# Kernel tuning notes

Measured on AMD Instinct MI355X. Metric: run time of the kernel, lower is better.

Reference implementation:

```python
import jax, jax.numpy as jnp
import numpy as np

CHEB_K = 2  # hops per support; stacked terms = 1 + 2*CHEB_K = 5


def setup_inputs() -> dict:
    key = jax.random.key(0)
    k1, k2, k3, k4, k5 = jax.random.split(key, 5)
    B, N, C, O, D = 16, 1024, 64, 64, 10
    return {
        "x": jax.random.normal(k1, (B, N, C), dtype=jnp.float32),
        "adj": jax.random.uniform(k2, (2, B, N, N), dtype=jnp.float32),
        "node_embedding": jax.random.normal(k3, (N, D), dtype=jnp.float32),
        "weights_pool": jax.random.normal(k4, (D, 2 * CHEB_K + 1, C, O), dtype=jnp.float32) * 0.1,
        "bias_pool": jax.random.normal(k5, (D, O), dtype=jnp.float32) * 0.1,
    }


def reference(x, adj, node_embedding, weights_pool, bias_pool):
    # k-hop graph aggregation over each of the 2 supports
    out = [x]
    for s in range(adj.shape[0]):
        a = adj[s]  # [B, N, N]
        x1 = x
        for _ in range(CHEB_K):
            x1 = jnp.einsum('bnm,bmc->bnc', a, x1)
            out.append(x1)
    x_g = jnp.stack(out, axis=2)  # [B, N, K, C] with K = 2*cheb_k+1 (already node-major)
    # per-node hypernetwork weights and bias from node embeddings
    weights = jnp.einsum('nd,dkio->nkio', node_embedding, weights_pool)  # [N, K, C, O]
    bias = node_embedding @ bias_pool  # [N, O]
    # per-node contraction over (K, C)
    return jnp.einsum('bnki,nkio->bno', x_g, weights) + bias
```

## Files before the change

### kernel.cpp

```cpp
#include <hip/hip_runtime.h>
#include <stdint.h>


typedef __attribute__((ext_vector_type(4))) float f32x4;
typedef __attribute__((ext_vector_type(2))) float f32x2;
typedef __attribute__((ext_vector_type(8))) short s16x8;
typedef __attribute__((ext_vector_type(8))) __bf16 bf16x8;

__device__ __forceinline__ unsigned short f2bf(float f) {
  union { float f; uint32_t u; } v; v.f = f;
  uint32_t r = v.u + 0x7FFFu + ((v.u >> 16) & 1u);
  return (unsigned short)(r >> 16);
}
__device__ __forceinline__ uint32_t pack2(float a, float b) {
  return (uint32_t)f2bf(a) | ((uint32_t)f2bf(b) << 16);
}

union FragU { s16x8 s; bf16x8 b; };

__global__ void transpose_x(const float* __restrict__ x,
                            unsigned short* __restrict__ XT0) {
  __shared__ unsigned short tl[64][72];
  const int b = blockIdx.y, n0 = blockIdx.x * 64;
  const int tid = threadIdx.x;
  {
    const int c4 = (tid & 15) * 4;
#pragma unroll
    for (int i = 0; i < 4; ++i) {
      const int row = (tid >> 4) + i * 16;
      f32x4 v = *(const f32x4*)(x + ((size_t)(b * 1024 + n0 + row)) * 64 + c4);
      *(uint32_t*)&tl[row][c4]     = pack2(v[0], v[1]);
      *(uint32_t*)&tl[row][c4 + 2] = pack2(v[2], v[3]);
    }
  }
  __syncthreads();
  {
    const int c = tid >> 2;
    const int nch = (tid & 3) * 16;
    s16x8 s0, s1;
#pragma unroll
    for (int j = 0; j < 8; ++j) {
      s0[j] = (short)tl[nch + j][c];
      s1[j] = (short)tl[nch + 8 + j][c];
    }
    unsigned short* p = XT0 + (size_t)(b * 64 + c) * 1024 + n0 + nch;
    *(s16x8*)p = s0;
    *(s16x8*)(p + 8) = s1;
  }
}

__global__ void transpose_wp(const float* __restrict__ wp,
                             float* __restrict__ wpT) {
  __shared__ float tl[64][65];
  const int d = blockIdx.y;
  const int ki0 = blockIdx.x * 64;
  const int tid = threadIdx.x;
  const float* src = wp + (size_t)d * 20480;
  {
    const int o4 = (tid & 15) * 4;
#pragma unroll
    for (int i = 0; i < 4; ++i) {
      const int row = (tid >> 4) + i * 16;
      f32x4 v = *(const f32x4*)(src + (size_t)(ki0 + row) * 64 + o4);
      tl[row][o4] = v[0]; tl[row][o4 + 1] = v[1];
      tl[row][o4 + 2] = v[2]; tl[row][o4 + 3] = v[3];
    }
  }
  __syncthreads();
  {
    const int o = tid >> 2;
    const int kch = (tid & 3) * 16;
    float* dst = wpT + (size_t)d * 20480 + (size_t)o * 320 + ki0 + kch;
#pragma unroll
    for (int u = 0; u < 4; ++u) {
      f32x4 v = { tl[kch + 4 * u][o], tl[kch + 4 * u + 1][o],
                  tl[kch + 4 * u + 2][o], tl[kch + 4 * u + 3][o] };
      *(f32x4*)(dst + 4 * u) = v;
    }
  }
}

__global__ __launch_bounds__(256) void wgen(const float* __restrict__ wpT,
                                            const float* __restrict__ emb,
                                            unsigned short* __restrict__ WT) {
  const int idx = blockIdx.x * 256 + threadIdx.x;
  const int n0 = blockIdx.y * 16;
  float wv[10];
#pragma unroll
  for (int d = 0; d < 10; ++d) wv[d] = wpT[(size_t)d * 20480 + idx];
#pragma unroll
  for (int g = 0; g < 16; ++g) {
    float a = 0.f;
#pragma unroll
    for (int d = 0; d < 10; ++d) a += emb[(n0 + g) * 10 + d] * wv[d];
    WT[(size_t)(n0 + g) * 20480 + idx] = f2bf(a);
  }
}

#define PF 4
__global__ __launch_bounds__(256, 2) void hop_kernel(
    const float* __restrict__ adj, const unsigned short* __restrict__ XTin,
    float* __restrict__ Xout, unsigned short* __restrict__ XTout,
    int xt_shared, int write_xt) {
  const int slice = blockIdx.y;
  const int b = slice & 15;
  const float* __restrict__ A = adj + (size_t)slice * (1024u * 1024u);
  const unsigned short* __restrict__ XT =
      XTin + (size_t)(xt_shared ? b : slice) * (64 * 1024);
  const int tid = threadIdx.x;
  const int wave = tid >> 6, lane = tid & 63;
  const int l15 = lane & 15, q = lane >> 4;
  const int rowbase = blockIdx.x * 64;
  const int arow = rowbase + wave * 16 + l15;
  const float* __restrict__ aptr = A + (size_t)arow * 1024 + q * 8;
  const unsigned short* __restrict__ bptr = XT + (size_t)l15 * 1024 + q * 8;

  f32x4 acc[4];
#pragma unroll
  for (int t = 0; t < 4; ++t) acc[t] = (f32x4){0.f, 0.f, 0.f, 0.f};

  f32x4 araw[PF][2];
  s16x8 braw[PF][4];

  auto load_stage = [&](int j, int k0) {
    araw[j][0] = *(const f32x4*)(aptr + k0);
    araw[j][1] = *(const f32x4*)(aptr + k0 + 4);
#pragma unroll
    for (int t = 0; t < 4; ++t)
      braw[j][t] = *(const s16x8*)(bptr + (size_t)t * (16 * 1024) + k0);
  };

#pragma unroll
  for (int j = 0; j < PF - 1; ++j) load_stage(j, j * 32);

  for (int it0 = 0; it0 < 32; it0 += PF) {
#pragma unroll
    for (int jj = 0; jj < PF; ++jj) {
      const int i = it0 + jj;
      const int kpre = (i + PF - 1) * 32;
      if (kpre < 1024) load_stage((jj + PF - 1) & (PF - 1), kpre);
      FragU af;
#pragma unroll
      for (int e = 0; e < 4; ++e) {
        af.s[e]     = (short)f2bf(araw[jj][0][e]);
        af.s[e + 4] = (short)f2bf(araw[jj][1][e]);
      }
#pragma unroll
      for (int t = 0; t < 4; ++t) {
        FragU bf; bf.s = braw[jj][t];
        acc[t] = __builtin_amdgcn_mfma_f32_16x16x32_bf16(af.b, bf.b, acc[t],
                                                         0, 0, 0);
      }
    }
  }

  __shared__ float tile[64][65];
#pragma unroll
  for (int t = 0; t < 4; ++t)
#pragma unroll
    for (int r = 0; r < 4; ++r)
      tile[wave * 16 + q * 4 + r][t * 16 + l15] = acc[t][r];
  __syncthreads();

  {
    const int row = tid >> 2;
    const int cb = (tid & 3) * 16;
    float* __restrict__ outp = Xout + (size_t)slice * (1024 * 64) +
                               (size_t)(rowbase + row) * 64 + cb;
#pragma unroll
    for (int u = 0; u < 4; ++u) {
      f32x4 v = { tile[row][cb + 4 * u], tile[row][cb + 4 * u + 1],
                  tile[row][cb + 4 * u + 2], tile[row][cb + 4 * u + 3] };
      *(f32x4*)(outp + 4 * u) = v;
    }
  }
  if (write_xt) {
    const int c = tid >> 2;
    const int nch = (tid & 3) * 16;
    unsigned short* __restrict__ xtp = XTout + (size_t)slice * (64 * 1024) +
                                       (size_t)c * 1024 + rowbase + nch;
    s16x8 s0, s1;
#pragma unroll
    for (int j = 0; j < 8; ++j) {
      s0[j] = (short)f2bf(tile[nch + j][c]);
      s1[j] = (short)f2bf(tile[nch + 8 + j][c]);
    }
    *(s16x8*)xtp = s0;
    *(s16x8*)(xtp + 8) = s1;
  }
}

__global__ __launch_bounds__(256, 2) void final_kernel(
    const float* __restrict__ x, const float* __restrict__ X1,
    const float* __restrict__ X2, const unsigned short* __restrict__ WT,
    const float* __restrict__ emb, const float* __restrict__ bias_pool,
    float* __restrict__ out) {
  __shared__ unsigned short xg[4][16][328];
  const int tid = threadIdx.x;
  const int node_base = blockIdx.x * 4;

  for (int u = tid; u < 10240; u += 256) {
    const int nd = u / 2560;
    int rem = u - nd * 2560;
    const int bb = rem / 160;
    const int kiu = rem - bb * 160;
    const int ki = kiu * 2;
    const int k = ki >> 6;
    const int c = ki & 63;
    const int nn = node_base + nd;
    const float* src;
    if (k == 0) {
      src = x + ((size_t)bb * 1024 + nn) * 64 + c;
    } else {
      const float* arr = (k == 1 || k == 3) ? X1 : X2;
      const int s = (k >= 3) ? 1 : 0;
      src = arr + ((size_t)(s * 16 + bb) * 1024 + nn) * 64 + c;
    }
    f32x2 v = *(const f32x2*)src;
    *(uint32_t*)&xg[nd][bb][ki] = pack2(v[0], v[1]);
  }
  __syncthreads();

  const int wave = tid >> 6, lane = tid & 63;
  const int l15 = lane & 15, q = lane >> 4;
  const int n = node_base + wave;
  f32x4 acc[4];
#pragma unroll
  for (int t = 0; t < 4; ++t) acc[t] = (f32x4){0.f, 0.f, 0.f, 0.f};

  const unsigned short* wt0 =
      WT + (size_t)n * 20480 + (size_t)l15 * 320 + q * 8;
#pragma unroll
  for (int ks = 0; ks < 10; ++ks) {
    const int k0 = ks * 32;
    FragU af;
    af.s = *(const s16x8*)&xg[wave][l15][k0 + q * 8];
#pragma unroll
    for (int t = 0; t < 4; ++t) {
      FragU bf;
      bf.s = *(const s16x8*)(wt0 + (size_t)t * (16 * 320) + k0);
      acc[t] = __builtin_amdgcn_mfma_f32_16x16x32_bf16(af.b, bf.b, acc[t],
                                                       0, 0, 0);
    }
  }

#pragma unroll
  for (int t = 0; t < 4; ++t) {
    const int o = t * 16 + l15;
    float bv = 0.f;
#pragma unroll
    for (int d = 0; d < 10; ++d)
      bv += emb[n * 10 + d] * bias_pool[d * 64 + o];
#pragma unroll
    for (int r = 0; r < 4; ++r) {
      const int bb = q * 4 + r;
      out[((size_t)bb * 1024 + n) * 64 + o] = acc[t][r] + bv;
    }
  }
}

extern "C" void kernel_launch(void* const* d_in, const int* in_sizes, int n_in,
                              void* d_out, int out_size, void* d_ws,
                              size_t ws_size, hipStream_t stream) {
  const float* x   = (const float*)d_in[0];
  const float* adj = (const float*)d_in[1];
  const float* emb = (const float*)d_in[2];
  const float* wp  = (const float*)d_in[3];
  const float* bp  = (const float*)d_in[4];
  float* out = (float*)d_out;

  char* ws = (char*)d_ws;
  unsigned short* XT0 = (unsigned short*)(ws);
  unsigned short* XT1 = (unsigned short*)(ws + ((size_t)2 << 20));
  float* X1  = (float*)(ws + ((size_t)6 << 20));
  float* X2  = (float*)(ws + ((size_t)14 << 20));
  float* wpT = (float*)(ws + ((size_t)22 << 20));
  unsigned short* WT = (unsigned short*)(ws + ((size_t)23 << 20));

  transpose_x<<<dim3(16, 16), dim3(256), 0, stream>>>(x, XT0);
  transpose_wp<<<dim3(5, 10), dim3(256), 0, stream>>>(wp, wpT);
  wgen<<<dim3(80, 64), dim3(256), 0, stream>>>(wpT, emb, WT);
  hop_kernel<<<dim3(16, 32), dim3(256), 0, stream>>>(adj, XT0, X1, XT1, 1, 1);
  hop_kernel<<<dim3(16, 32), dim3(256), 0, stream>>>(adj, XT1, X2,
                                                     (unsigned short*)nullptr,
                                                     0, 0);
  final_kernel<<<dim3(256), dim3(256), 0, stream>>>(x, X1, X2, WT, emb, bp,
                                                    out);
}
```

Measured before the change: 314.0 us.

## Stage hop-kernel operands through LDS with async global-to-LDS double buffering

The hop kernel stops prefetching A and XT tiles straight into registers with a 4-deep register pipeline. It now copies 64-wide K tiles into double-buffered, XOR-swizzled shared memory using global_load_lds and reads the MFMA fragments back from LDS. The aim is to lower register pressure and make the adjacency stream more coalesced, at the cost of a barrier per K tile. Separately, wgen now processes two outputs per thread with vectorized loads and packed bf16 stores, and its grid is halved to match.

```diff
diff --git a/kernel.cpp b/kernel.cpp
--- a/kernel.cpp
+++ b/kernel.cpp
@@ -17,6 +17,12 @@
 }
 
 union FragU { s16x8 s; bf16x8 b; };
+
+__device__ __forceinline__ void async_cp16(const void* g, void* l) {
+  __builtin_amdgcn_global_load_lds(
+      (const __attribute__((address_space(1))) void*)g,
+      (__attribute__((address_space(3))) void*)l, 16, 0, 0);
+}
 
 __global__ void transpose_x(const float* __restrict__ x,
                             unsigned short* __restrict__ XT0) {
@@ -83,25 +89,30 @@
 __global__ __launch_bounds__(256) void wgen(const float* __restrict__ wpT,
                                             const float* __restrict__ emb,
                                             unsigned short* __restrict__ WT) {
-  const int idx = blockIdx.x * 256 + threadIdx.x;
+  const int idx = (blockIdx.x * 256 + threadIdx.x) * 2;
   const int n0 = blockIdx.y * 16;
-  float wv[10];
-#pragma unroll
-  for (int d = 0; d < 10; ++d) wv[d] = wpT[(size_t)d * 20480 + idx];
+  f32x2 wv[10];
+#pragma unroll
+  for (int d = 0; d < 10; ++d)
+    wv[d] = *(const f32x2*)(wpT + (size_t)d * 20480 + idx);
 #pragma unroll
   for (int g = 0; g < 16; ++g) {
-    float a = 0.f;
-#pragma unroll
-    for (int d = 0; d < 10; ++d) a += emb[(n0 + g) * 10 + d] * wv[d];
-    WT[(size_t)(n0 + g) * 20480 + idx] = f2bf(a);
-  }
-}
-
-#define PF 4
+    float a0 = 0.f, a1 = 0.f;
+#pragma unroll
+    for (int d = 0; d < 10; ++d) {
+      const float e = emb[(n0 + g) * 10 + d];
+      a0 += e * wv[d][0];
+      a1 += e * wv[d][1];
+    }
+    *(uint32_t*)(WT + (size_t)(n0 + g) * 20480 + idx) = pack2(a0, a1);
+  }
+}
+
 __global__ __launch_bounds__(256, 2) void hop_kernel(
     const float* __restrict__ adj, const unsigned short* __restrict__ XTin,
     float* __restrict__ Xout, unsigned short* __restrict__ XTout,
     int xt_shared, int write_xt) {
+  __shared__ __align__(16) char smem[2 * (16384 + 8192)];
   const int slice = blockIdx.y;
   const int b = slice & 15;
   const float* __restrict__ A = adj + (size_t)slice * (1024u * 1024u);
@@ -111,55 +122,82 @@
   const int wave = tid >> 6, lane = tid & 63;
   const int l15 = lane & 15, q = lane >> 4;
   const int rowbase = blockIdx.x * 64;
-  const int arow = rowbase + wave * 16 + l15;
-  const float* __restrict__ aptr = A + (size_t)arow * 1024 + q * 8;
-  const unsigned short* __restrict__ bptr = XT + (size_t)l15 * 1024 + q * 8;
+
+  int arow[4], acol[4];
+#pragma unroll
+  for (int i = 0; i < 4; ++i) {
+    const int r = wave * 16 + i * 4 + (lane >> 4);
+    arow[i] = r;
+    acol[i] = ((lane & 15) ^ (r & 7)) * 4;
+  }
+  int bc[2], bcol[2];
+#pragma unroll
+  for (int i = 0; i < 2; ++i) {
+    const int c = wave * 16 + i * 8 + (lane >> 3);
+    bc[i] = c;
+    bcol[i] = ((lane & 7) ^ (c & 7)) * 8;
+  }
+
+  float* const Ab0 = (float*)smem;
+  float* const Ab1 = (float*)(smem + 24576);
+  unsigned short* const Bb0 = (unsigned short*)(smem + 16384);
+  unsigned short* const Bb1 = (unsigned short*)(smem + 24576 + 16384);
+
+  auto issue = [&](int k0, int s) {
+    float* Abuf = s ? Ab1 : Ab0;
+    unsigned short* Bbuf = s ? Bb1 : Bb0;
+#pragma unroll
+    for (int i = 0; i < 4; ++i)
+      async_cp16(A + (size_t)(rowbase + arow[i]) * 1024 + k0 + acol[i],
+                 Abuf + (size_t)(wave * 16 + i * 4) * 64);
+#pragma unroll
+    for (int i = 0; i < 2; ++i)
+      async_cp16(XT + (size_t)bc[i] * 1024 + k0 + bcol[i],
+                 Bbuf + (size_t)(wave * 16 + i * 8) * 64);
+  };
 
   f32x4 acc[4];
 #pragma unroll
   for (int t = 0; t < 4; ++t) acc[t] = (f32x4){0.f, 0.f, 0.f, 0.f};
 
-  f32x4 araw[PF][2];
-  s16x8 braw[PF][4];
-
-  auto load_stage = [&](int j, int k0) {
-    araw[j][0] = *(const f32x4*)(aptr + k0);
-    araw[j][1] = *(const f32x4*)(aptr + k0 + 4);
-#pragma unroll
-    for (int t = 0; t < 4; ++t)
-      braw[j][t] = *(const s16x8*)(bptr + (size_t)t * (16 * 1024) + k0);
-  };
-
-#pragma unroll
-  for (int j = 0; j < PF - 1; ++j) load_stage(j, j * 32);
-
-  for (int it0 = 0; it0 < 32; it0 += PF) {
-#pragma unroll
-    for (int jj = 0; jj < PF; ++jj) {
-      const int i = it0 + jj;
-      const int kpre = (i + PF - 1) * 32;
-      if (kpre < 1024) load_stage((jj + PF - 1) & (PF - 1), kpre);
+  issue(0, 0);
+  const int r = wave * 16 + l15;
+  const int rx = r & 7;
+  for (int kt = 0; kt < 16; ++kt) {
+    const int cur = kt & 1;
+    __syncthreads();
+    if (kt + 1 < 16) issue((kt + 1) * 64, cur ^ 1);
+    const float* Abuf = cur ? Ab1 : Ab0;
+    const unsigned short* Bbuf = cur ? Bb1 : Bb0;
+#pragma unroll
+    for (int h = 0; h < 2; ++h) {
+      const int j0 = h * 8 + q * 2;
+      f32x4 c0 = *(const f32x4*)(Abuf + r * 64 + ((j0) ^ rx) * 4);
+      f32x4 c1 = *(const f32x4*)(Abuf + r * 64 + ((j0 + 1) ^ rx) * 4);
       FragU af;
 #pragma unroll
       for (int e = 0; e < 4; ++e) {
-        af.s[e]     = (short)f2bf(araw[jj][0][e]);
-        af.s[e + 4] = (short)f2bf(araw[jj][1][e]);
+        af.s[e]     = (short)f2bf(c0[e]);
+        af.s[e + 4] = (short)f2bf(c1[e]);
       }
+      const int pc = (h * 4 + q) ^ (l15 & 7);
 #pragma unroll
       for (int t = 0; t < 4; ++t) {
-        FragU bf; bf.s = braw[jj][t];
+        FragU bf;
+        bf.s = *(const s16x8*)(Bbuf + (t * 16 + l15) * 64 + pc * 8);
         acc[t] = __builtin_amdgcn_mfma_f32_16x16x32_bf16(af.b, bf.b, acc[t],
                                                          0, 0, 0);
       }
     }
   }
 
-  __shared__ float tile[64][65];
+  __syncthreads();
+  float (*tile)[65] = (float(*)[65])smem;
 #pragma unroll
   for (int t = 0; t < 4; ++t)
 #pragma unroll
-    for (int r = 0; r < 4; ++r)
-      tile[wave * 16 + q * 4 + r][t * 16 + l15] = acc[t][r];
+    for (int rr = 0; rr < 4; ++rr)
+      tile[wave * 16 + q * 4 + rr][t * 16 + l15] = acc[t][rr];
   __syncthreads();
 
   {
@@ -252,9 +290,9 @@
     for (int d = 0; d < 10; ++d)
       bv += emb[n * 10 + d] * bias_pool[d * 64 + o];
 #pragma unroll
-    for (int r = 0; r < 4; ++r) {
-      const int bb = q * 4 + r;
-      out[((size_t)bb * 1024 + n) * 64 + o] = acc[t][r] + bv;
+    for (int rr = 0; rr < 4; ++rr) {
+      const int bb = q * 4 + rr;
+      out[((size_t)bb * 1024 + n) * 64 + o] = acc[t][rr] + bv;
     }
   }
 }
@@ -279,7 +317,7 @@
 
   transpose_x<<<dim3(16, 16), dim3(256), 0, stream>>>(x, XT0);
   transpose_wp<<<dim3(5, 10), dim3(256), 0, stream>>>(wp, wpT);
-  wgen<<<dim3(80, 64), dim3(256), 0, stream>>>(wpT, emb, WT);
+  wgen<<<dim3(40, 64), dim3(256), 0, stream>>>(wpT, emb, WT);
   hop_kernel<<<dim3(16, 32), dim3(256), 0, stream>>>(adj, XT0, X1, XT1, 1, 1);
   hop_kernel<<<dim3(16, 32), dim3(256), 0, stream>>>(adj, XT1, X2,
                                                      (unsigned short*)nullptr,
```

New measurement: 279.1 us. 11.1% less time.
